# Kernel tuning notes

Hardware: AMD Instinct MI355X
Metric: run time of the kernel (lower is better)

## Reference

```python
import jax, jax.numpy as jnp
import numpy as np

VOCAB = 1000
MAX_T = 1000  # max_episode_length
L = 64        # instruction length


def _uniform(key, shape, fan_in, fan_out):
    bound = float(np.sqrt(6.0 / (fan_in + fan_out)))
    return jax.random.uniform(key, shape, jnp.float32, -bound, bound)


def setup_inputs() -> dict:
    key = jax.random.key(0)
    ks = jax.random.split(key, 20)
    s = float(1.0 / np.sqrt(256.0))
    inp = {}
    inp['x'] = jax.random.normal(ks[0], (1, 400), jnp.float32)
    inp['input_inst'] = jax.random.randint(ks[1], (1, L), 0, VOCAB)
    inp['tx'] = jax.random.randint(ks[2], (1,), 0, MAX_T + 1)
    inp['hx'] = jax.random.normal(ks[3], (1, 256), jnp.float32) * 0.1
    inp['cx'] = jax.random.normal(ks[4], (1, 256), jnp.float32) * 0.1
    inp['img1_w'] = _uniform(ks[5], (128, 400), 400, 128); inp['img1_b'] = jnp.zeros((128,), jnp.float32)
    inp['img2_w'] = _uniform(ks[6], (128, 128), 128, 128); inp['img2_b'] = jnp.zeros((128,), jnp.float32)
    inp['img3_w'] = _uniform(ks[7], (128, 128), 128, 128); inp['img3_b'] = jnp.zeros((128,), jnp.float32)
    inp['emb'] = jax.random.normal(ks[8], (VOCAB, 32), jnp.float32)
    inp['gru_wi'] = jax.random.uniform(ks[9], (768, 32), jnp.float32, -s, s)
    inp['gru_wh'] = jax.random.uniform(ks[10], (768, 256), jnp.float32, -s, s)
    inp['gru_bi'] = jnp.zeros((768,), jnp.float32); inp['gru_bh'] = jnp.zeros((768,), jnp.float32)
    inp['attn_w'] = _uniform(ks[11], (128, 256), 256, 128); inp['attn_b'] = jnp.zeros((128,), jnp.float32)
    inp['time_emb'] = jax.random.normal(ks[12], (MAX_T + 1, 32), jnp.float32)
    inp['lin_w'] = _uniform(ks[13], (256, 128), 128, 256); inp['lin_b'] = jnp.zeros((256,), jnp.float32)
    inp['lstm_wi'] = jax.random.uniform(ks[14], (1024, 256), jnp.float32, -s, s)
    inp['lstm_wh'] = jax.random.uniform(ks[15], (1024, 256), jnp.float32, -s, s)
    inp['lstm_bi'] = jnp.zeros((1024,), jnp.float32); inp['lstm_bh'] = jnp.zeros((1024,), jnp.float32)
    inp['crit_w'] = jax.random.normal(ks[16], (1, 288), jnp.float32) * 0.06
    inp['crit_b'] = jnp.zeros((1,), jnp.float32)
    inp['act_w'] = jax.random.normal(ks[17], (4, 288), jnp.float32) * 0.01
    inp['act_b'] = jnp.zeros((4,), jnp.float32)
    return inp


def _linear(x, w, b):
    return x @ w.T + b


def reference(x, input_inst, tx, hx, cx,
              img1_w, img1_b, img2_w, img2_b, img3_w, img3_b,
              emb, gru_wi, gru_wh, gru_bi, gru_bh,
              attn_w, attn_b, time_emb, lin_w, lin_b,
              lstm_wi, lstm_wh, lstm_bi, lstm_bh,
              crit_w, crit_b, act_w, act_b):
    # image MLP: 400 -> 128 -> 128 -> 128
    h = jax.nn.relu(_linear(x.reshape(x.shape[0], -1), img1_w, img1_b))
    h = jax.nn.relu(_linear(h, img2_w, img2_b))
    x_image_rep = jax.nn.relu(_linear(h, img3_w, img3_b))  # (1,128)

    # GRU encoder over instruction tokens (torch gate order: r, z, n)
    emb_seq = emb[input_inst[0]]  # (L, 32)

    def gru_step(hg, e):
        gi = gru_wi @ e + gru_bi        # (768,)
        gh = gru_wh @ hg + gru_bh       # (768,)
        ir, iz, i_n = jnp.split(gi, 3)
        hr, hz, hn = jnp.split(gh, 3)
        r = jax.nn.sigmoid(ir + hr)
        z = jax.nn.sigmoid(iz + hz)
        n = jnp.tanh(i_n + r * hn)
        return (1.0 - z) * n + z * hg, None

    h_enc, _ = jax.lax.scan(gru_step, jnp.zeros((256,), x.dtype), emb_seq)
    x_instr_rep = h_enc[None, :]  # (1,256)

    # gated attention fusion
    x_attention = jax.nn.sigmoid(_linear(x_instr_rep, attn_w, attn_b))  # (1,128)
    fused = x_image_rep * x_attention
    fused = jax.nn.relu(_linear(fused, lin_w, lin_b))  # (1,256)

    # LSTMCell (torch gate order: i, f, g, o)
    gates = fused @ lstm_wi.T + lstm_bi + hx @ lstm_wh.T + lstm_bh  # (1,1024)
    i_g, f_g, g_g, o_g = jnp.split(gates, 4, axis=1)
    c_new = jax.nn.sigmoid(f_g) * cx + jax.nn.sigmoid(i_g) * jnp.tanh(g_g)
    h_new = jax.nn.sigmoid(o_g) * jnp.tanh(c_new)

    t_emb = time_emb[tx].reshape(-1, 32)  # (1,32)
    feat = jnp.concatenate([h_new, t_emb], axis=1)  # (1,288)
    return _linear(feat, crit_w, crit_b), _linear(feat, act_w, act_b), h_new, c_new
```

## Files before the change

kernel.cpp:

```cpp
#include <hip/hip_runtime.h>
#include <math.h>


typedef __fp16 h2 __attribute__((ext_vector_type(2)));
typedef __fp16 h8 __attribute__((ext_vector_type(8)));
typedef float  f4 __attribute__((ext_vector_type(4)));

#define WS_IMG    0
#define WS_GATESH 128
#define WS_FUSED  1152
#define WS_GI     1408
#define WS_REGW   50560

__device__ __forceinline__ float dot4(const float4 a, const float4 b){
  return a.x*b.x + a.y*b.y + a.z*b.z + a.w*b.w;
}
__device__ __forceinline__ float sigm(float x){ return 1.f/(1.f+expf(-x)); }

#define P0(v) __builtin_shufflevector(v,v,0,1)
#define P1(v) __builtin_shufflevector(v,v,2,3)
#define P2(v) __builtin_shufflevector(v,v,4,5)
#define P3(v) __builtin_shufflevector(v,v,6,7)
#define PK(a,b) __builtin_amdgcn_cvt_pkrtz(a,b)
#define FD(w,e,acc) __builtin_amdgcn_fdot2(w,e,acc,false)

__global__ __launch_bounds__(256) void a3c_pre(
    const float* __restrict__ x,
    const float* __restrict__ i1w, const float* __restrict__ i1b,
    const float* __restrict__ i2w, const float* __restrict__ i2b,
    const float* __restrict__ i3w, const float* __restrict__ i3b,
    const float* __restrict__ hx,  const float* __restrict__ lwh,
    const float* __restrict__ lbh,
    const int*   __restrict__ tx,  const float* __restrict__ temb,
    const float* __restrict__ cw,  const float* __restrict__ cb,
    const float* __restrict__ acw, const float* __restrict__ acb,
    const int*   __restrict__ inst, const float* __restrict__ emb,
    const float* __restrict__ gwi,  const float* __restrict__ gbi,
    const float* __restrict__ gwh,
    float* __restrict__ ws, float* __restrict__ out)
{
  const int b = blockIdx.x;
  const int t = threadIdx.x;

  if (b == 0) {
    __shared__ __align__(16) float x_lds[400];
    __shared__ __align__(16) float h1[128];
    __shared__ __align__(16) float h2s[128];
    x_lds[t] = x[t];
    if (t < 144) x_lds[256+t] = x[256+t];
    __syncthreads();
    {
      const int o = t>>1, half = t&1;
      const float4* wr = (const float4*)(i1w + o*400 + half*200);
      const float4* xr = (const float4*)(x_lds + half*200);
      float acc = 0.f;
      #pragma unroll 5
      for (int k=0;k<50;++k) acc += dot4(wr[k], xr[k]);
      acc += __shfl_down(acc, 1, 2);
      if (half == 0) h1[o] = fmaxf(acc + i1b[o], 0.f);
    }
    __syncthreads();
    if (t < 128){
      const float4* wr = (const float4*)(i2w + t*128);
      const float4* h4 = (const float4*)h1;
      float acc = i2b[t];
      #pragma unroll 8
      for (int k=0;k<32;++k) acc += dot4(wr[k], h4[k]);
      h2s[t] = fmaxf(acc, 0.f);
    }
    __syncthreads();
    if (t < 128){
      const float4* wr = (const float4*)(i3w + t*128);
      const float4* h4 = (const float4*)h2s;
      float acc = i3b[t];
      #pragma unroll 8
      for (int k=0;k<32;++k) acc += dot4(wr[k], h4[k]);
      ws[WS_IMG + t] = fmaxf(acc, 0.f);
    }

  } else if (b <= 4) {
    __shared__ __align__(16) float hx_lds[256];
    hx_lds[t] = hx[t];
    __syncthreads();
    const int R = (b-1)*256 + t;
    const float4* wr = (const float4*)(lwh + R*256);
    const float4* h4 = (const float4*)hx_lds;
    float acc = lbh[R];
    #pragma unroll 8
    for (int k=0;k<64;++k) acc += dot4(wr[k], h4[k]);
    ws[WS_GATESH + R] = acc;

  } else if (b == 5) {
    if (t < 64){
      float tv = 0.f;
      if (t < 32) tv = temb[tx[0]*32 + t];
      #pragma unroll
      for (int o=0;o<5;++o){
        const float* wrow = (o==0) ? cw : (acw + (o-1)*288);
        float pr = (t < 32) ? tv*wrow[256+t] : 0.f;
        #pragma unroll
        for (int off=16; off; off>>=1) pr += __shfl_down(pr, off, 32);
        if (t == 0) out[o] = pr + ((o==0) ? cb[0] : acb[o-1]);
      }
    }

  } else if (b < 198) {
    const int idx = (b-6)*256 + t;
    const int s = idx / 768;
    const int r = idx - s*768;
    const float4* wr = (const float4*)(gwi + r*32);
    const float4* er = (const float4*)(emb + inst[s]*32);
    float acc = gbi[r];
    #pragma unroll
    for (int k=0;k<8;++k) acc += dot4(wr[k], er[k]);
    ws[WS_GI + idx] = acc;

  } else {
    const int d = (b-198)*256 + t;
    const int e = d << 1;
    const int tt = e / 192;
    int rem = e - tt*192;
    const int rho = rem >> 5; rem &= 31;
    const int c = rem >> 3;
    const int el = rem & 7;
    const int row = 6*(tt>>3) + rho;
    const int col = ((tt&7)<<5) + (c<<3) + el;
    ((h2*)(ws + WS_REGW))[d] = PK(gwh[row*256+col], gwh[row*256+col+1]);
  }
}

__global__ __attribute__((amdgpu_flat_work_group_size(1024,1024)))
void a3c_scan(
    const float* __restrict__ gbh,
    const float* __restrict__ aw,  const float* __restrict__ ab,
    const float* __restrict__ lnw, const float* __restrict__ lnb,
    float* __restrict__ ws)
{
  const int t = threadIdx.x;
  const int o = t >> 3, i = t & 7;

  __shared__ __align__(16) __fp16 h16[256];
  __shared__ float h32[256];
  __shared__ float pp[768*9];
  __shared__ float bhl[768];
  __shared__ float gil[2][768];
  __shared__ __align__(16) float f0[128];

  if (t < 768){ bhl[t] = gbh[t]; gil[0][t] = ws[WS_GI + t]; }
  if (t < 256){ h16[t] = (__fp16)0.f; h32[t] = 0.f; }

  const f4* rw = (const f4*)(ws + WS_REGW) + t*24;
  f4 W00=rw[0],  W01=rw[1],  W02=rw[2],  W03=rw[3];
  f4 W10=rw[4],  W11=rw[5],  W12=rw[6],  W13=rw[7];
  f4 W20=rw[8],  W21=rw[9],  W22=rw[10], W23=rw[11];
  f4 W30=rw[12], W31=rw[13], W32=rw[14], W33=rw[15];
  f4 W40=rw[16], W41=rw[17], W42=rw[18], W43=rw[19];
  f4 W50=rw[20], W51=rw[21], W52=rw[22], W53=rw[23];
  #define PIN(v) asm volatile("" : "+v"(v))
  PIN(W00);PIN(W01);PIN(W02);PIN(W03);PIN(W10);PIN(W11);PIN(W12);PIN(W13);
  PIN(W20);PIN(W21);PIN(W22);PIN(W23);PIN(W30);PIN(W31);PIN(W32);PIN(W33);
  PIN(W40);PIN(W41);PIN(W42);PIN(W43);PIN(W50);PIN(W51);PIN(W52);PIN(W53);
  #undef PIN
  __syncthreads();

  const int pbase = o*6;
  int cur = 0;
  for (int s=0; s<64; ++s){
    float gnx = 0.f;
    if (t < 768) gnx = ws[WS_GI + ((s<63)?(s+1):s)*768 + t];

    float a0=0.f,a1=0.f,a2=0.f,a3=0.f,a4=0.f,a5=0.f;
    #define CHUNK(c) { \
      const h8 hv = *(const h8*)(h16 + (i<<5) + ((c)<<3)); h8 w; \
      w=__builtin_bit_cast(h8,W0##c); \
      a0=FD(P0(w),P0(hv),a0); a0=FD(P1(w),P1(hv),a0); \
      a0=FD(P2(w),P2(hv),a0); a0=FD(P3(w),P3(hv),a0); \
      w=__builtin_bit_cast(h8,W1##c); \
      a1=FD(P0(w),P0(hv),a1); a1=FD(P1(w),P1(hv),a1); \
      a1=FD(P2(w),P2(hv),a1); a1=FD(P3(w),P3(hv),a1); \
      w=__builtin_bit_cast(h8,W2##c); \
      a2=FD(P0(w),P0(hv),a2); a2=FD(P1(w),P1(hv),a2); \
      a2=FD(P2(w),P2(hv),a2); a2=FD(P3(w),P3(hv),a2); \
      w=__builtin_bit_cast(h8,W3##c); \
      a3=FD(P0(w),P0(hv),a3); a3=FD(P1(w),P1(hv),a3); \
      a3=FD(P2(w),P2(hv),a3); a3=FD(P3(w),P3(hv),a3); \
      w=__builtin_bit_cast(h8,W4##c); \
      a4=FD(P0(w),P0(hv),a4); a4=FD(P1(w),P1(hv),a4); \
      a4=FD(P2(w),P2(hv),a4); a4=FD(P3(w),P3(hv),a4); \
      w=__builtin_bit_cast(h8,W5##c); \
      a5=FD(P0(w),P0(hv),a5); a5=FD(P1(w),P1(hv),a5); \
      a5=FD(P2(w),P2(hv),a5); a5=FD(P3(w),P3(hv),a5); }
    CHUNK(0) CHUNK(1) CHUNK(2) CHUNK(3)
    #undef CHUNK

    pp[(pbase+0)*9+i]=a0; pp[(pbase+1)*9+i]=a1; pp[(pbase+2)*9+i]=a2;
    pp[(pbase+3)*9+i]=a3; pp[(pbase+4)*9+i]=a4; pp[(pbase+5)*9+i]=a5;
    if (t < 768) gil[cur^1][t] = gnx;
    __syncthreads();
    if (t < 256){
      const float* pr = pp + t*9;
      const float* pz = pp + (256+t)*9;
      const float* pn = pp + (512+t)*9;
      float sr=bhl[t], sz=bhl[256+t], sn=bhl[512+t];
      #pragma unroll
      for (int k=0;k<8;++k){ sr+=pr[k]; sz+=pz[k]; sn+=pn[k]; }
      const float rr = sigm(gil[cur][t]       + sr);
      const float zz = sigm(gil[cur][256 + t] + sz);
      const float nn = tanhf(gil[cur][512 + t] + rr*sn);
      const float hv = (1.f - zz)*nn + zz*h32[t];
      h32[t] = hv;
      h16[t] = (__fp16)hv;
    }
    cur ^= 1;
    __syncthreads();
  }

  if (t < 128){
    const float4* wr = (const float4*)(aw + t*256);
    const float4* h4 = (const float4*)h32;
    float acc = ab[t];
    #pragma unroll 8
    for (int k=0;k<64;++k) acc += dot4(wr[k], h4[k]);
    f0[t] = ws[WS_IMG + t] * sigm(acc);
  }
  __syncthreads();
  if (t < 256){
    const float4* wr = (const float4*)(lnw + t*128);
    const float4* h4 = (const float4*)f0;
    float acc = lnb[t];
    #pragma unroll 8
    for (int k=0;k<32;++k) acc += dot4(wr[k], h4[k]);
    ws[WS_FUSED + t] = fmaxf(acc, 0.f);
  }
}

__global__ __launch_bounds__(256) void a3c_post(
    const float* __restrict__ lwi, const float* __restrict__ lbi,
    const float* __restrict__ cx,
    const float* __restrict__ cw,  const float* __restrict__ acw,
    float* __restrict__ ws, float* __restrict__ out)
{
  const int p = blockIdx.x;
  const int t = threadIdx.x;
  __shared__ __align__(16) float fused_lds[256];
  __shared__ float gv[256];
  __shared__ float hh[64];
  fused_lds[t] = ws[WS_FUSED + t];
  __syncthreads();
  const int g = t>>6, ul = t&63;
  const int R = (g<<8) + p*64 + ul;
  const float4* wr = (const float4*)(lwi + R*256);
  const float4* f4p = (const float4*)fused_lds;
  float acc = ws[WS_GATESH + R] + lbi[R];
  #pragma unroll 8
  for (int k=0;k<64;++k) acc += dot4(wr[k], f4p[k]);
  gv[t] = acc;
  __syncthreads();
  if (t < 64){
    const int u2 = p*64 + t;
    const float iv = gv[t], fv = gv[64+t], gg = gv[128+t], ov = gv[192+t];
    const float c = sigm(fv)*cx[u2] + sigm(iv)*tanhf(gg);
    const float h = sigm(ov)*tanhf(c);
    out[5   + u2] = h;
    out[261 + u2] = c;
    hh[t] = h;
  }
  __syncthreads();
  if (t < 64){
    #pragma unroll
    for (int o=0;o<5;++o){
      const float* wrow = (o==0) ? cw : (acw + (o-1)*288);
      float pr = hh[t]*wrow[p*64 + t];
      #pragma unroll
      for (int off=32; off; off>>=1) pr += __shfl_down(pr, off, 64);
      if (t == 0) atomicAdd(out + o, pr);
    }
  }
}

extern "C" void kernel_launch(void* const* d_in, const int* in_sizes, int n_in,
                              void* d_out, int out_size, void* d_ws, size_t ws_size,
                              hipStream_t stream) {
  (void)in_sizes; (void)n_in; (void)out_size; (void)ws_size;
  const float* x    = (const float*)d_in[0];
  const int*   inst = (const int*)  d_in[1];
  const int*   tx   = (const int*)  d_in[2];
  const float* hx   = (const float*)d_in[3];
  const float* cx   = (const float*)d_in[4];
  const float* i1w  = (const float*)d_in[5];
  const float* i1b  = (const float*)d_in[6];
  const float* i2w  = (const float*)d_in[7];
  const float* i2b  = (const float*)d_in[8];
  const float* i3w  = (const float*)d_in[9];
  const float* i3b  = (const float*)d_in[10];
  const float* emb  = (const float*)d_in[11];
  const float* gwi  = (const float*)d_in[12];
  const float* gwh  = (const float*)d_in[13];
  const float* gbi  = (const float*)d_in[14];
  const float* gbh  = (const float*)d_in[15];
  const float* aw   = (const float*)d_in[16];
  const float* ab   = (const float*)d_in[17];
  const float* temb = (const float*)d_in[18];
  const float* lnw  = (const float*)d_in[19];
  const float* lnb  = (const float*)d_in[20];
  const float* lwi  = (const float*)d_in[21];
  const float* lwh  = (const float*)d_in[22];
  const float* lbi  = (const float*)d_in[23];
  const float* lbh  = (const float*)d_in[24];
  const float* cw   = (const float*)d_in[25];
  const float* cb   = (const float*)d_in[26];
  const float* acw  = (const float*)d_in[27];
  const float* acb  = (const float*)d_in[28];
  float* ws  = (float*)d_ws;
  float* out = (float*)d_out;

  a3c_pre <<<582, 256, 0, stream>>>(x, i1w, i1b, i2w, i2b, i3w, i3b,
                                    hx, lwh, lbh, tx, temb, cw, cb, acw, acb,
                                    inst, emb, gwi, gbi, gwh, ws, out);
  a3c_scan<<<1, 1024, 0, stream>>>(gbh, aw, ab, lnw, lnb, ws);
  a3c_post<<<4, 256, 0, stream>>>(lwi, lbi, cx, cw, acw, ws, out);
}
```

Measured before the change: 125.8 us.

## Give each scan thread a full hidden unit's three GRU rows in registers

```diff
diff --git a/kernel.cpp b/kernel.cpp
--- a/kernel.cpp
+++ b/kernel.cpp
@@ -117,19 +117,16 @@
 
   } else {
     const int d = (b-198)*256 + t;
-    const int e = d << 1;
-    const int tt = e / 192;
-    int rem = e - tt*192;
-    const int rho = rem >> 5; rem &= 31;
-    const int c = rem >> 3;
-    const int el = rem & 7;
-    const int row = 6*(tt>>3) + rho;
-    const int col = ((tt&7)<<5) + (c<<3) + el;
+    const int ft = d >> 2, e2 = d & 3;
+    const int f = ft >> 8, tt = ft & 255;
+    const int g = f >> 5,  c = f & 31;
+    const int row = (g<<8) + tt;
+    const int col = (c<<3) + (e2<<1);
     ((h2*)(ws + WS_REGW))[d] = PK(gwh[row*256+col], gwh[row*256+col+1]);
   }
 }
 
-__global__ __attribute__((amdgpu_flat_work_group_size(1024,1024)))
+__global__ __launch_bounds__(256) __attribute__((amdgpu_waves_per_eu(1, 1)))
 void a3c_scan(
     const float* __restrict__ gbh,
     const float* __restrict__ aw,  const float* __restrict__ ab,
@@ -137,81 +134,65 @@
     float* __restrict__ ws)
 {
   const int t = threadIdx.x;
-  const int o = t >> 3, i = t & 7;
-
   __shared__ __align__(16) __fp16 h16[256];
-  __shared__ float h32[256];
-  __shared__ float pp[768*9];
-  __shared__ float bhl[768];
-  __shared__ float gil[2][768];
+  __shared__ __align__(16) float h32[256];
   __shared__ __align__(16) float f0[128];
 
-  if (t < 768){ bhl[t] = gbh[t]; gil[0][t] = ws[WS_GI + t]; }
-  if (t < 256){ h16[t] = (__fp16)0.f; h32[t] = 0.f; }
-
-  const f4* rw = (const f4*)(ws + WS_REGW) + t*24;
-  f4 W00=rw[0],  W01=rw[1],  W02=rw[2],  W03=rw[3];
-  f4 W10=rw[4],  W11=rw[5],  W12=rw[6],  W13=rw[7];
-  f4 W20=rw[8],  W21=rw[9],  W22=rw[10], W23=rw[11];
-  f4 W30=rw[12], W31=rw[13], W32=rw[14], W33=rw[15];
-  f4 W40=rw[16], W41=rw[17], W42=rw[18], W43=rw[19];
-  f4 W50=rw[20], W51=rw[21], W52=rw[22], W53=rw[23];
-  #define PIN(v) asm volatile("" : "+v"(v))
-  PIN(W00);PIN(W01);PIN(W02);PIN(W03);PIN(W10);PIN(W11);PIN(W12);PIN(W13);
-  PIN(W20);PIN(W21);PIN(W22);PIN(W23);PIN(W30);PIN(W31);PIN(W32);PIN(W33);
-  PIN(W40);PIN(W41);PIN(W42);PIN(W43);PIN(W50);PIN(W51);PIN(W52);PIN(W53);
-  #undef PIN
-  __syncthreads();
-
-  const int pbase = o*6;
-  int cur = 0;
+  f4 w0[32], w1[32], w2[32];
+  {
+    const f4* src = (const f4*)(ws + WS_REGW);
+    #pragma unroll
+    for (int c=0;c<32;++c) w0[c] = src[(c     )*256 + t];
+    #pragma unroll
+    for (int c=0;c<32;++c) w1[c] = src[(32 + c)*256 + t];
+    #pragma unroll
+    for (int c=0;c<32;++c) w2[c] = src[(64 + c)*256 + t];
+    #pragma unroll
+    for (int c=0;c<32;++c){
+      asm volatile("" : "+v"(w0[c]));
+      asm volatile("" : "+v"(w1[c]));
+      asm volatile("" : "+v"(w2[c]));
+    }
+  }
+  const float bh0 = gbh[t], bh1 = gbh[256+t], bh2 = gbh[512+t];
+  h16[t] = (__fp16)0.f;
+  h32[t] = 0.f;
+  float g0 = ws[WS_GI + t];
+  float g1 = ws[WS_GI + 256 + t];
+  float g2 = ws[WS_GI + 512 + t];
+  __syncthreads();
+
   for (int s=0; s<64; ++s){
-    float gnx = 0.f;
-    if (t < 768) gnx = ws[WS_GI + ((s<63)?(s+1):s)*768 + t];
-
-    float a0=0.f,a1=0.f,a2=0.f,a3=0.f,a4=0.f,a5=0.f;
-    #define CHUNK(c) { \
-      const h8 hv = *(const h8*)(h16 + (i<<5) + ((c)<<3)); h8 w; \
-      w=__builtin_bit_cast(h8,W0##c); \
-      a0=FD(P0(w),P0(hv),a0); a0=FD(P1(w),P1(hv),a0); \
-      a0=FD(P2(w),P2(hv),a0); a0=FD(P3(w),P3(hv),a0); \
-      w=__builtin_bit_cast(h8,W1##c); \
-      a1=FD(P0(w),P0(hv),a1); a1=FD(P1(w),P1(hv),a1); \
-      a1=FD(P2(w),P2(hv),a1); a1=FD(P3(w),P3(hv),a1); \
-      w=__builtin_bit_cast(h8,W2##c); \
-      a2=FD(P0(w),P0(hv),a2); a2=FD(P1(w),P1(hv),a2); \
-      a2=FD(P2(w),P2(hv),a2); a2=FD(P3(w),P3(hv),a2); \
-      w=__builtin_bit_cast(h8,W3##c); \
-      a3=FD(P0(w),P0(hv),a3); a3=FD(P1(w),P1(hv),a3); \
-      a3=FD(P2(w),P2(hv),a3); a3=FD(P3(w),P3(hv),a3); \
-      w=__builtin_bit_cast(h8,W4##c); \
-      a4=FD(P0(w),P0(hv),a4); a4=FD(P1(w),P1(hv),a4); \
-      a4=FD(P2(w),P2(hv),a4); a4=FD(P3(w),P3(hv),a4); \
-      w=__builtin_bit_cast(h8,W5##c); \
-      a5=FD(P0(w),P0(hv),a5); a5=FD(P1(w),P1(hv),a5); \
-      a5=FD(P2(w),P2(hv),a5); a5=FD(P3(w),P3(hv),a5); }
-    CHUNK(0) CHUNK(1) CHUNK(2) CHUNK(3)
-    #undef CHUNK
-
-    pp[(pbase+0)*9+i]=a0; pp[(pbase+1)*9+i]=a1; pp[(pbase+2)*9+i]=a2;
-    pp[(pbase+3)*9+i]=a3; pp[(pbase+4)*9+i]=a4; pp[(pbase+5)*9+i]=a5;
-    if (t < 768) gil[cur^1][t] = gnx;
-    __syncthreads();
-    if (t < 256){
-      const float* pr = pp + t*9;
-      const float* pz = pp + (256+t)*9;
-      const float* pn = pp + (512+t)*9;
-      float sr=bhl[t], sz=bhl[256+t], sn=bhl[512+t];
-      #pragma unroll
-      for (int k=0;k<8;++k){ sr+=pr[k]; sz+=pz[k]; sn+=pn[k]; }
-      const float rr = sigm(gil[cur][t]       + sr);
-      const float zz = sigm(gil[cur][256 + t] + sz);
-      const float nn = tanhf(gil[cur][512 + t] + rr*sn);
-      const float hv = (1.f - zz)*nn + zz*h32[t];
-      h32[t] = hv;
-      h16[t] = (__fp16)hv;
-    }
-    cur ^= 1;
+    const int nx = (s<63) ? (s+1) : s;
+    const float n0 = ws[WS_GI + nx*768 + t];
+    const float n1 = ws[WS_GI + nx*768 + 256 + t];
+    const float n2 = ws[WS_GI + nx*768 + 512 + t];
+
+    float a0=0.f,b0=0.f, a1=0.f,b1=0.f, a2=0.f,b2=0.f;
+    #pragma unroll
+    for (int c=0;c<32;++c){
+      const h8 hv = *(const h8*)(h16 + (c<<3));
+      const h8 u0 = __builtin_bit_cast(h8, w0[c]);
+      const h8 u1 = __builtin_bit_cast(h8, w1[c]);
+      const h8 u2 = __builtin_bit_cast(h8, w2[c]);
+      a0=FD(P0(u0),P0(hv),a0); b0=FD(P1(u0),P1(hv),b0);
+      a0=FD(P2(u0),P2(hv),a0); b0=FD(P3(u0),P3(hv),b0);
+      a1=FD(P0(u1),P0(hv),a1); b1=FD(P1(u1),P1(hv),b1);
+      a1=FD(P2(u1),P2(hv),a1); b1=FD(P3(u1),P3(hv),b1);
+      a2=FD(P0(u2),P0(hv),a2); b2=FD(P1(u2),P1(hv),b2);
+      a2=FD(P2(u2),P2(hv),a2); b2=FD(P3(u2),P3(hv),b2);
+    }
+    const float sr = a0 + b0 + bh0;
+    const float sz = a1 + b1 + bh1;
+    const float sn = a2 + b2 + bh2;
+    const float rr = sigm(g0 + sr);
+    const float zz = sigm(g1 + sz);
+    const float nn = tanhf(g2 + rr*sn);
+    const float hv_ = (1.f - zz)*nn + zz*h32[t];
+    __syncthreads();
+    h32[t] = hv_;
+    h16[t] = (__fp16)hv_;
+    g0 = n0; g1 = n1; g2 = n2;
     __syncthreads();
   }
 
@@ -224,7 +205,7 @@
     f0[t] = ws[WS_IMG + t] * sigm(acc);
   }
   __syncthreads();
-  if (t < 256){
+  {
     const float4* wr = (const float4*)(lnw + t*128);
     const float4* h4 = (const float4*)f0;
     float acc = lnb[t];
@@ -317,6 +298,6 @@
   a3c_pre <<<582, 256, 0, stream>>>(x, i1w, i1b, i2w, i2b, i3w, i3b,
                                     hx, lwh, lbh, tx, temb, cw, cb, acw, acb,
                                     inst, emb, gwi, gbi, gwh, ws, out);
-  a3c_scan<<<1, 1024, 0, stream>>>(gbh, aw, ab, lnw, lnb, ws);
+  a3c_scan<<<1, 256, 0, stream>>>(gbh, aw, ab, lnw, lnb, ws);
   a3c_post<<<4, 256, 0, stream>>>(lwi, lbi, cx, cw, acw, ws, out);
 }
```

Measured after the change: 190.9 us. 1.52x slower.

## Fuse LSTM post kernel into scan kernel with flag-based inter-block sync

Applied to the files above, without the earlier changes.

```diff
diff --git a/kernel.cpp b/kernel.cpp
--- a/kernel.cpp
+++ b/kernel.cpp
@@ -11,6 +11,7 @@
 #define WS_FUSED  1152
 #define WS_GI     1408
 #define WS_REGW   50560
+#define WS_FLAG   148864
 
 __device__ __forceinline__ float dot4(const float4 a, const float4 b){
   return a.x*b.x + a.y*b.y + a.z*b.z + a.w*b.w;
@@ -91,6 +92,7 @@
     ws[WS_GATESH + R] = acc;
 
   } else if (b == 5) {
+    if (t == 64) ((int*)(ws + WS_FLAG))[0] = 0;
     if (t < 64){
       float tv = 0.f;
       if (t < 32) tv = temb[tx[0]*32 + t];
@@ -134,9 +136,69 @@
     const float* __restrict__ gbh,
     const float* __restrict__ aw,  const float* __restrict__ ab,
     const float* __restrict__ lnw, const float* __restrict__ lnb,
-    float* __restrict__ ws)
+    const float* __restrict__ lwi, const float* __restrict__ lbi,
+    const float* __restrict__ cx,
+    const float* __restrict__ cw,  const float* __restrict__ acw,
+    float* __restrict__ ws, float* __restrict__ out)
 {
+  const int b = blockIdx.x;
   const int t = threadIdx.x;
+  int* F = (int*)(ws + WS_FLAG);
+
+  if (b > 0){
+    __shared__ __align__(16) float fused_lds[256];
+    __shared__ float gv[256];
+    __shared__ float hh[64];
+    const int p = b - 1;
+    const int tt = t & 255, q = t >> 8;
+    const int g = tt >> 6, ul = tt & 63;
+    const int R = (g<<8) + p*64 + ul;
+    {
+      const float4* wr4 = (const float4*)(lwi + R*256) + q*16;
+      float pf = 0.f;
+      #pragma unroll
+      for (int k=0;k<16;++k){ float4 w = wr4[k]; pf += w.x+w.y+w.z+w.w; }
+      asm volatile("" :: "v"(pf));
+    }
+    if (t == 0){
+      while (__hip_atomic_load(F, __ATOMIC_ACQUIRE,
+                               __HIP_MEMORY_SCOPE_AGENT) == 0){}
+    }
+    __syncthreads();
+    if (t < 256) fused_lds[t] = ws[WS_FUSED + t];
+    __syncthreads();
+    if (t < 256){
+      const float4* wr = (const float4*)(lwi + R*256);
+      const float4* f4p = (const float4*)fused_lds;
+      float acc = ws[WS_GATESH + R] + lbi[R];
+      #pragma unroll 8
+      for (int k=0;k<64;++k) acc += dot4(wr[k], f4p[k]);
+      gv[t] = acc;
+    }
+    __syncthreads();
+    if (t < 64){
+      const int u2 = p*64 + t;
+      const float iv = gv[t], fv = gv[64+t], gg = gv[128+t], ov = gv[192+t];
+      const float c = sigm(fv)*cx[u2] + sigm(iv)*tanhf(gg);
+      const float h = sigm(ov)*tanhf(c);
+      out[5   + u2] = h;
+      out[261 + u2] = c;
+      hh[t] = h;
+    }
+    __syncthreads();
+    if (t < 64){
+      #pragma unroll
+      for (int o=0;o<5;++o){
+        const float* wrow = (o==0) ? cw : (acw + (o-1)*288);
+        float pr = hh[t]*wrow[p*64 + t];
+        #pragma unroll
+        for (int off=32; off; off>>=1) pr += __shfl_down(pr, off, 64);
+        if (t == 0) atomicAdd(out + o, pr);
+      }
+    }
+    return;
+  }
+
   const int o = t >> 3, i = t & 7;
 
   __shared__ __align__(16) __fp16 h16[256];
@@ -232,49 +294,10 @@
     for (int k=0;k<32;++k) acc += dot4(wr[k], h4[k]);
     ws[WS_FUSED + t] = fmaxf(acc, 0.f);
   }
-}
-
-__global__ __launch_bounds__(256) void a3c_post(
-    const float* __restrict__ lwi, const float* __restrict__ lbi,
-    const float* __restrict__ cx,
-    const float* __restrict__ cw,  const float* __restrict__ acw,
-    float* __restrict__ ws, float* __restrict__ out)
-{
-  const int p = blockIdx.x;
-  const int t = threadIdx.x;
-  __shared__ __align__(16) float fused_lds[256];
-  __shared__ float gv[256];
-  __shared__ float hh[64];
-  fused_lds[t] = ws[WS_FUSED + t];
   __syncthreads();
-  const int g = t>>6, ul = t&63;
-  const int R = (g<<8) + p*64 + ul;
-  const float4* wr = (const float4*)(lwi + R*256);
-  const float4* f4p = (const float4*)fused_lds;
-  float acc = ws[WS_GATESH + R] + lbi[R];
-  #pragma unroll 8
-  for (int k=0;k<64;++k) acc += dot4(wr[k], f4p[k]);
-  gv[t] = acc;
-  __syncthreads();
-  if (t < 64){
-    const int u2 = p*64 + t;
-    const float iv = gv[t], fv = gv[64+t], gg = gv[128+t], ov = gv[192+t];
-    const float c = sigm(fv)*cx[u2] + sigm(iv)*tanhf(gg);
-    const float h = sigm(ov)*tanhf(c);
-    out[5   + u2] = h;
-    out[261 + u2] = c;
-    hh[t] = h;
-  }
-  __syncthreads();
-  if (t < 64){
-    #pragma unroll
-    for (int o=0;o<5;++o){
-      const float* wrow = (o==0) ? cw : (acw + (o-1)*288);
-      float pr = hh[t]*wrow[p*64 + t];
-      #pragma unroll
-      for (int off=32; off; off>>=1) pr += __shfl_down(pr, off, 64);
-      if (t == 0) atomicAdd(out + o, pr);
-    }
+  if (t == 0){
+    __threadfence();
+    __hip_atomic_store(F, 1, __ATOMIC_RELEASE, __HIP_MEMORY_SCOPE_AGENT);
   }
 }
 
@@ -317,6 +340,6 @@
   a3c_pre <<<582, 256, 0, stream>>>(x, i1w, i1b, i2w, i2b, i3w, i3b,
                                     hx, lwh, lbh, tx, temb, cw, cb, acw, acb,
                                     inst, emb, gwi, gbi, gwh, ws, out);
-  a3c_scan<<<1, 1024, 0, stream>>>(gbh, aw, ab, lnw, lnb, ws);
-  a3c_post<<<4, 256, 0, stream>>>(lwi, lbi, cx, cw, acw, ws, out);
+  a3c_scan<<<5, 1024, 0, stream>>>(gbh, aw, ab, lnw, lnb,
+                                   lwi, lbi, cx, cw, acw, ws, out);
 }
```

Result: no change. 127.7 us (+1.5%).
